# Kernel optimization log

Hardware: AMD Instinct MI355X
Metric: run time of the kernel (lower is better)

Reference implementation:

```python
import jax, jax.numpy as jnp
import numpy as np

N, NIN, NOUT = 8192, 512, 512


def setup_inputs() -> dict:
    key = jax.random.key(0)
    k1, k2, k3 = jax.random.split(key, 3)
    H = jax.random.normal(k1, (N, NIN), dtype=jnp.float32)
    adj_matrix = jax.random.uniform(k2, (N, N), dtype=jnp.float32)
    W = jax.random.normal(k3, (NOUT, NIN), dtype=jnp.float32) / np.sqrt(NIN)
    b = jnp.zeros((NOUT,), dtype=jnp.float32)
    return {"H": H, "adj_matrix": adj_matrix, "W": W, "b": b}


def reference(H, adj_matrix, W, b):
    n = adj_matrix.shape[0]
    # adj + I (self-loops)
    A = adj_matrix + jnp.eye(n, dtype=adj_matrix.dtype)
    # column degrees (torch.sum(dim=0))
    deg = jnp.sum(A, axis=0)
    d = deg ** -0.5
    d = jnp.where(jnp.isinf(d), 0.0, d)
    # D^-1/2 A D^-1/2 implemented as elementwise row/col rescale (same math as diag matmuls)
    A = d[:, None] * A * d[None, :]
    # message passing + linear (torch Linear: x @ W.T + b) + tanh
    Hm = A @ H  # [N, nin]
    out = jnp.tanh(Hm @ W.T + b)
    return out
```

## Files before the change

kernel.cpp:

```cpp
#include <hip/hip_runtime.h>
#include <hip/hip_bf16.h>

#define N_NODES 8192
#define N_IN 512
#define N_OUT 512

typedef __bf16 bf16;
typedef __bf16 bf16x4 __attribute__((ext_vector_type(4)));
typedef __bf16 bf16x8 __attribute__((ext_vector_type(8)));
typedef float f32x4 __attribute__((ext_vector_type(4)));

__device__ __forceinline__ void gload16(const void* g, void* l) {
  __builtin_amdgcn_global_load_lds((const __attribute__((address_space(1))) void*)g,
                                   (__attribute__((address_space(3))) void*)l, 16, 0, 0);
}

#define WAITVM(N) asm volatile("s_waitcnt vmcnt(" #N ")" ::: "memory")

__global__ __launch_bounds__(256) void k_colsum_cvt(const float* __restrict__ adj,
                                                    bf16* __restrict__ adjb,
                                                    float* __restrict__ partial) {
  const int tid  = threadIdx.x;
  const int col0 = blockIdx.x * 1024 + tid * 4;
  const int row0 = blockIdx.y * 64;
  float s0 = 0.f, s1 = 0.f, s2 = 0.f, s3 = 0.f;
#pragma unroll 4
  for (int r = 0; r < 64; ++r) {
    const float4 v = *reinterpret_cast<const float4*>(adj + (size_t)(row0 + r) * N_NODES + col0);
    s0 += v.x; s1 += v.y; s2 += v.z; s3 += v.w;
    bf16x4 o = { (bf16)v.x, (bf16)v.y, (bf16)v.z, (bf16)v.w };
    *reinterpret_cast<bf16x4*>(adjb + (size_t)(row0 + r) * N_NODES + col0) = o;
  }
  float4 ps = { s0, s1, s2, s3 };
  *reinterpret_cast<float4*>(partial + (size_t)blockIdx.y * N_NODES + col0) = ps;
}

__global__ __launch_bounds__(256) void k_dvec(const float* __restrict__ partial,
                                              float* __restrict__ dv) {
  const int j = blockIdx.x * 256 + threadIdx.x;
  float s = 1.0f;
#pragma unroll 8
  for (int p = 0; p < 128; ++p) s += partial[(size_t)p * N_NODES + j];
  dv[j] = rsqrtf(s);
}

__global__ __launch_bounds__(256) void k_hst(const float* __restrict__ H,
                                             const float* __restrict__ dv,
                                             bf16* __restrict__ Hst) {
  __shared__ float t[64][65];
  const int tid = threadIdx.x;
  const int j0 = blockIdx.x * 64;
  const int k0 = blockIdx.y * 64;
  const int rr = tid >> 4;
  const int cc = (tid & 15) * 4;
#pragma unroll
  for (int p = 0; p < 4; ++p) {
    const int r = p * 16 + rr;
    const float d = dv[j0 + r];
    float4 v = *reinterpret_cast<const float4*>(H + (size_t)(j0 + r) * N_IN + k0 + cc);
    t[r][cc + 0] = v.x * d; t[r][cc + 1] = v.y * d;
    t[r][cc + 2] = v.z * d; t[r][cc + 3] = v.w * d;
  }
  __syncthreads();
#pragma unroll
  for (int p = 0; p < 4; ++p) {
    const int kr = p * 16 + rr;
    bf16x4 o = { (bf16)t[cc + 0][kr], (bf16)t[cc + 1][kr],
                 (bf16)t[cc + 2][kr], (bf16)t[cc + 3][kr] };
    *reinterpret_cast<bf16x4*>(Hst + (size_t)(k0 + kr) * N_NODES + j0 + cc) = o;
  }
}

__global__ __launch_bounds__(256) void k_wcvt(const float* __restrict__ W, bf16* __restrict__ Wb) {
  const int i = (blockIdx.x * 256 + threadIdx.x) * 4;
  float4 v = *reinterpret_cast<const float4*>(W + i);
  bf16x4 o = { (bf16)v.x, (bf16)v.y, (bf16)v.z, (bf16)v.w };
  *reinterpret_cast<bf16x4*>(Wb + i) = o;
}

template<int KDIM, int NSPLIT, int EPI>
__global__ __launch_bounds__(256, 2) void k_gemm(
    const bf16* __restrict__ A, const bf16* __restrict__ B,
    const float* __restrict__ bias, float* __restrict__ outf) {
  constexpr int KSEG = KDIM / NSPLIT;
  constexpr int NT = KSEG / 64;
  constexpr int NBLK = 256 * NSPLIT;
  __shared__ __attribute__((aligned(128))) char lds[2 * 32768];

  const int bid = blockIdx.x;
  const int logical = (bid & 7) * (NBLK / 8) + (bid >> 3);
  const int split = logical & (NSPLIT - 1);
  const int tile = logical / NSPLIT;
  const int bm0 = (tile >> 2) * 128;
  const int bn0 = (tile & 3) * 128;

  const int tid = threadIdx.x;
  const int wid = tid >> 6;
  const int lane = tid & 63;
  const int wr = wid & 1, wc = wid >> 1;

  const int srow = tid >> 3;
  const int scol = ((tid & 7) ^ (srow & 7)) << 3;
  const size_t a_src = (size_t)(bm0 + srow) * KDIM + (size_t)split * KSEG + scol;
  const size_t b_src = (size_t)(bn0 + srow) * KDIM + (size_t)split * KSEG + scol;

  const int frow = lane & 15;
  const int fk = lane >> 4;
  const int swz = (lane & 7) << 4;
  const int a_row_byte = (wr * 64 + frow) * 128;
  const int b_row_byte = 16384 + (wc * 64 + frow) * 128;

  f32x4 acc[4][4] = {};

  auto stage = [&](int t) {
    char* lbase = lds + (t & 1) * 32768;
    const bf16* ag = A + a_src + (size_t)t * 64;
    const bf16* bg = B + b_src + (size_t)t * 64;
#pragma unroll
    for (int ch = 0; ch < 4; ++ch) {
      gload16(ag + (size_t)(ch * 32) * KDIM, lbase + ch * 4096 + wid * 1024);
      gload16(bg + (size_t)(ch * 32) * KDIM, lbase + 16384 + ch * 4096 + wid * 1024);
    }
  };

  auto compute = [&](int t) {
    const char* lbase = lds + (t & 1) * 32768;
#pragma unroll
    for (int kk = 0; kk < 2; ++kk) {
      const int colb = (kk * 64 + fk * 16) ^ swz;
      bf16x8 av[4], bv[4];
#pragma unroll
      for (int m = 0; m < 4; ++m)
        av[m] = *reinterpret_cast<const bf16x8*>(lbase + a_row_byte + m * 2048 + colb);
#pragma unroll
      for (int n = 0; n < 4; ++n)
        bv[n] = *reinterpret_cast<const bf16x8*>(lbase + b_row_byte + n * 2048 + colb);
#pragma unroll
      for (int m = 0; m < 4; ++m)
#pragma unroll
        for (int n = 0; n < 4; ++n)
          acc[m][n] = __builtin_amdgcn_mfma_f32_16x16x32_bf16(av[m], bv[n], acc[m][n], 0, 0, 0);
    }
  };

  stage(0);
#pragma unroll 1
  for (int t = 0; t < NT - 1; ++t) {
    stage(t + 1);
    WAITVM(8);
    __builtin_amdgcn_s_barrier();
    asm volatile("" ::: "memory");
    compute(t);
    asm volatile("" ::: "memory");
    __builtin_amdgcn_s_barrier();
  }
  WAITVM(0);
  __builtin_amdgcn_s_barrier();
  compute(NT - 1);

#pragma unroll
  for (int m = 0; m < 4; ++m) {
#pragma unroll
    for (int j = 0; j < 4; ++j) {
      const int grow = bm0 + wr * 64 + m * 16 + (lane >> 4) * 4 + j;
      if constexpr (EPI == 2) {
        float* prow = outf + (size_t)split * ((size_t)N_NODES * N_IN) + (size_t)grow * N_IN;
#pragma unroll
        for (int n = 0; n < 4; ++n) {
          const int gcol = bn0 + wc * 64 + n * 16 + (lane & 15);
          prow[gcol] = acc[m][n][j];
        }
      } else {
        float* orow = outf + (size_t)grow * N_OUT;
#pragma unroll
        for (int n = 0; n < 4; ++n) {
          const int gcol = bn0 + wc * 64 + n * 16 + (lane & 15);
          float v = acc[m][n][j] + bias[gcol];
          v = fminf(fmaxf(v, -15.f), 15.f);
          const float e = __expf(2.f * v);
          orow[gcol] = (e - 1.f) / (e + 1.f);
        }
      }
    }
  }
}

__global__ __launch_bounds__(256) void k_red(const float* __restrict__ P,
                                             const float* __restrict__ H,
                                             const float* __restrict__ dv,
                                             bf16* __restrict__ Hm) {
  const int t = blockIdx.x * 256 + threadIdx.x;
  const int row = t >> 7;
  const int col = (t & 127) << 2;
  const size_t off = (size_t)row * N_IN + col;
  const float d = dv[row];
  const float d2 = d * d;
  const float4 p0 = *reinterpret_cast<const float4*>(P + off);
  const float4 p1 = *reinterpret_cast<const float4*>(P + (size_t)N_NODES * N_IN + off);
  const float4 h  = *reinterpret_cast<const float4*>(H + off);
  bf16x4 o = { (bf16)(d * (p0.x + p1.x) + d2 * h.x),
               (bf16)(d * (p0.y + p1.y) + d2 * h.y),
               (bf16)(d * (p0.z + p1.z) + d2 * h.z),
               (bf16)(d * (p0.w + p1.w) + d2 * h.w) };
  *reinterpret_cast<bf16x4*>(Hm + off) = o;
}

extern "C" void kernel_launch(void* const* d_in, const int* in_sizes, int n_in,
                              void* d_out, int out_size, void* d_ws, size_t ws_size,
                              hipStream_t stream) {
  const float* H   = (const float*)d_in[0];
  const float* adj = (const float*)d_in[1];
  const float* W   = (const float*)d_in[2];
  const float* b   = (const float*)d_in[3];
  float* out = (float*)d_out;
  char* ws = (char*)d_ws;

  bf16*  adjb = (bf16*)(ws);
  bf16*  Hst  = (bf16*)(ws + 134217728);
  bf16*  Hm   = (bf16*)(ws + 142606336);
  bf16*  Wb   = (bf16*)(ws + 150994944);
  float* part = (float*)(ws + 151519232);
  float* dv   = (float*)(ws + 155713536);
  float* P    = (float*)(ws + 155746304);

  k_colsum_cvt<<<dim3(8, 128), 256, 0, stream>>>(adj, adjb, part);
  k_dvec<<<32, 256, 0, stream>>>(part, dv);
  k_hst<<<dim3(128, 8), 256, 0, stream>>>(H, dv, Hst);
  k_wcvt<<<256, 256, 0, stream>>>(W, Wb);
  k_gemm<8192, 2, 2><<<512, 256, 0, stream>>>(adjb, Hst, nullptr, P);
  k_red<<<4096, 256, 0, stream>>>(P, H, dv, Hm);
  k_gemm<512, 1, 1><<<256, 256, 0, stream>>>(Hm, Wb, b, out);
}
```

Measured before the change: 208.3 us.

## Use 256x256-tile 4-stage pipelined GEMM with 4-way split-K for adjacency matmul

Replaces the 128x128 double-buffered big GEMM with a 512-thread kernel computing 256x256 tiles, using a 4-deep LDS ring with BK=32, setprio around the MFMA block, and 4-way split-K. The larger tile halves the global/LDS traffic per FLOP and the deeper pipeline is meant to hide load latency better. The reduction kernel now sums four partial buffers, which doubles the fp32 partial traffic written and read. LDS use is 128KB per block, so occupancy is limited.

After: 199.2 us. -4.3%, faster.

```diff
diff --git a/kernel.cpp b/kernel.cpp
--- a/kernel.cpp
+++ b/kernel.cpp
@@ -78,6 +78,100 @@
   *reinterpret_cast<bf16x4*>(Wb + i) = o;
 }
 
+template<int KDIM, int NSPLIT>
+__global__ __launch_bounds__(512, 2) void k_gemm256(
+    const bf16* __restrict__ A, const bf16* __restrict__ B, float* __restrict__ P) {
+  constexpr int KSEG = KDIM / NSPLIT;
+  constexpr int NT = KSEG / 32;
+  constexpr int NTN = 2;
+  constexpr int NBLK = 32 * NTN * NSPLIT;
+  __shared__ __attribute__((aligned(128))) char lds[4 * 32768];
+
+  const int bid = blockIdx.x;
+  const int logical = (bid & 7) * (NBLK / 8) + (bid >> 3);
+  const int split = logical / (32 * NTN);
+  const int rem = logical % (32 * NTN);
+  const int bm0 = (rem >> 1) * 256;
+  const int bn0 = (rem & 1) * 256;
+
+  const int tid = threadIdx.x;
+  const int lane = tid & 63;
+  const int wid = tid >> 6;
+  const int wr = wid >> 2;
+  const int wc = wid & 3;
+
+  const int srow = tid >> 2;
+  const int scol = ((tid & 3) ^ ((srow >> 1) & 3)) << 3;
+  const size_t a_src = (size_t)(bm0 + srow) * KDIM + (size_t)split * KSEG + scol;
+  const size_t b_src = (size_t)(bn0 + srow) * KDIM + (size_t)split * KSEG + scol;
+
+  const int frow = lane & 15;
+  const int fk = lane >> 4;
+  const int colb = (fk << 4) ^ (((frow >> 1) & 3) << 4);
+  const int a_base = (wr * 128 + frow) * 64 + colb;
+  const int b_base = 16384 + (wc * 64 + frow) * 64 + colb;
+
+  f32x4 acc[8][4] = {};
+
+  auto stage = [&](int t) {
+    char* lbase = lds + (t & 3) * 32768;
+    const bf16* ag = A + a_src + (size_t)t * 32;
+    const bf16* bg = B + b_src + (size_t)t * 32;
+    gload16(ag,                        lbase +         tid * 16);
+    gload16(ag + (size_t)128 * KDIM,   lbase +  8192 + tid * 16);
+    gload16(bg,                        lbase + 16384 + tid * 16);
+    gload16(bg + (size_t)128 * KDIM,   lbase + 24576 + tid * 16);
+  };
+
+  auto compute = [&](int t) {
+    const char* lbase = lds + (t & 3) * 32768;
+    bf16x8 av[8], bv[4];
+#pragma unroll
+    for (int m = 0; m < 8; ++m)
+      av[m] = *reinterpret_cast<const bf16x8*>(lbase + a_base + m * 1024);
+#pragma unroll
+    for (int n = 0; n < 4; ++n)
+      bv[n] = *reinterpret_cast<const bf16x8*>(lbase + b_base + n * 1024);
+    __builtin_amdgcn_s_setprio(1);
+#pragma unroll
+    for (int m = 0; m < 8; ++m)
+#pragma unroll
+      for (int n = 0; n < 4; ++n)
+        acc[m][n] = __builtin_amdgcn_mfma_f32_16x16x32_bf16(av[m], bv[n], acc[m][n], 0, 0, 0);
+    __builtin_amdgcn_s_setprio(0);
+  };
+
+  stage(0); stage(1); stage(2);
+#pragma unroll 1
+  for (int t = 0; t < NT; ++t) {
+    if (t + 3 < NT) stage(t + 3);
+    const int ahead = NT - 1 - t;
+    if (ahead >= 3)      WAITVM(12);
+    else if (ahead == 2) WAITVM(8);
+    else if (ahead == 1) WAITVM(4);
+    else                 WAITVM(0);
+    __builtin_amdgcn_s_barrier();
+    asm volatile("" ::: "memory");
+    compute(t);
+    asm volatile("" ::: "memory");
+    __builtin_amdgcn_s_barrier();
+  }
+
+#pragma unroll
+  for (int m = 0; m < 8; ++m) {
+#pragma unroll
+    for (int j = 0; j < 4; ++j) {
+      const int grow = bm0 + wr * 128 + m * 16 + (lane >> 4) * 4 + j;
+      float* prow = P + (size_t)split * ((size_t)N_NODES * N_IN) + (size_t)grow * N_IN;
+#pragma unroll
+      for (int n = 0; n < 4; ++n) {
+        const int gcol = bn0 + wc * 64 + n * 16 + (lane & 15);
+        prow[gcol] = acc[m][n][j];
+      }
+    }
+  }
+}
+
 template<int KDIM, int NSPLIT, int EPI>
 __global__ __launch_bounds__(256, 2) void k_gemm(
     const bf16* __restrict__ A, const bf16* __restrict__ B,
@@ -163,23 +257,14 @@
 #pragma unroll
     for (int j = 0; j < 4; ++j) {
       const int grow = bm0 + wr * 64 + m * 16 + (lane >> 4) * 4 + j;
-      if constexpr (EPI == 2) {
-        float* prow = outf + (size_t)split * ((size_t)N_NODES * N_IN) + (size_t)grow * N_IN;
-#pragma unroll
-        for (int n = 0; n < 4; ++n) {
-          const int gcol = bn0 + wc * 64 + n * 16 + (lane & 15);
-          prow[gcol] = acc[m][n][j];
-        }
-      } else {
-        float* orow = outf + (size_t)grow * N_OUT;
-#pragma unroll
-        for (int n = 0; n < 4; ++n) {
-          const int gcol = bn0 + wc * 64 + n * 16 + (lane & 15);
-          float v = acc[m][n][j] + bias[gcol];
-          v = fminf(fmaxf(v, -15.f), 15.f);
-          const float e = __expf(2.f * v);
-          orow[gcol] = (e - 1.f) / (e + 1.f);
-        }
+      float* orow = outf + (size_t)grow * N_OUT;
+#pragma unroll
+      for (int n = 0; n < 4; ++n) {
+        const int gcol = bn0 + wc * 64 + n * 16 + (lane & 15);
+        float v = acc[m][n][j] + bias[gcol];
+        v = fminf(fmaxf(v, -15.f), 15.f);
+        const float e = __expf(2.f * v);
+        orow[gcol] = (e - 1.f) / (e + 1.f);
       }
     }
   }
@@ -193,15 +278,18 @@
   const int row = t >> 7;
   const int col = (t & 127) << 2;
   const size_t off = (size_t)row * N_IN + col;
+  constexpr size_t S = (size_t)N_NODES * N_IN;
   const float d = dv[row];
   const float d2 = d * d;
   const float4 p0 = *reinterpret_cast<const float4*>(P + off);
-  const float4 p1 = *reinterpret_cast<const float4*>(P + (size_t)N_NODES * N_IN + off);
+  const float4 p1 = *reinterpret_cast<const float4*>(P + S + off);
+  const float4 p2 = *reinterpret_cast<const float4*>(P + 2 * S + off);
+  const float4 p3 = *reinterpret_cast<const float4*>(P + 3 * S + off);
   const float4 h  = *reinterpret_cast<const float4*>(H + off);
-  bf16x4 o = { (bf16)(d * (p0.x + p1.x) + d2 * h.x),
-               (bf16)(d * (p0.y + p1.y) + d2 * h.y),
-               (bf16)(d * (p0.z + p1.z) + d2 * h.z),
-               (bf16)(d * (p0.w + p1.w) + d2 * h.w) };
+  bf16x4 o = { (bf16)(d * ((p0.x + p1.x) + (p2.x + p3.x)) + d2 * h.x),
+               (bf16)(d * ((p0.y + p1.y) + (p2.y + p3.y)) + d2 * h.y),
+               (bf16)(d * ((p0.z + p1.z) + (p2.z + p3.z)) + d2 * h.z),
+               (bf16)(d * ((p0.w + p1.w) + (p2.w + p3.w)) + d2 * h.w) };
   *reinterpret_cast<bf16x4*>(Hm + off) = o;
 }
 
@@ -227,7 +315,7 @@
   k_dvec<<<32, 256, 0, stream>>>(part, dv);
   k_hst<<<dim3(128, 8), 256, 0, stream>>>(H, dv, Hst);
   k_wcvt<<<256, 256, 0, stream>>>(W, Wb);
-  k_gemm<8192, 2, 2><<<512, 256, 0, stream>>>(adjb, Hst, nullptr, P);
+  k_gemm256<8192, 4><<<256, 512, 0, stream>>>(adjb, Hst, P);
   k_red<<<4096, 256, 0, stream>>>(P, H, dv, Hm);
   k_gemm<512, 1, 1><<<256, 256, 0, stream>>>(Hm, Wb, b, out);
 }
```
